# Performance work log

Measured on AMD Instinct MI355X. Metric: run time of the kernel, lower is better.

The kernel has to match this reference:

```python
import jax, jax.numpy as jnp
import numpy as np

N = 50000      # nodes
E = 800000     # edges (avg degree 16)
IN = 128       # in_feats
HID = 32       # hidden_feats per head
H = 4          # num_heads
NEG_SLOPE = 0.2


def setup_inputs() -> dict:
    key = jax.random.key(0)
    ks = jax.random.split(key, 13)
    x = jax.random.normal(ks[0], (N, IN), jnp.float32)
    src = jax.random.randint(ks[1], (E,), 0, N, jnp.int32)
    dst = jax.random.randint(ks[2], (E,), 0, N, jnp.int32)

    def lin(k, fi, fo):
        return jax.random.normal(k, (fi, fo), jnp.float32) * (1.0 / np.sqrt(fi))

    # conv1: IN -> H*HID
    W1 = lin(ks[3], IN, H * HID)
    al1 = jax.random.normal(ks[4], (H, HID), jnp.float32) * 0.1
    ar1 = jax.random.normal(ks[5], (H, HID), jnp.float32) * 0.1
    b1 = jnp.zeros((H, HID), jnp.float32)
    # conv2: H*HID -> H*HID
    W2 = lin(ks[6], H * HID, H * HID)
    al2 = jax.random.normal(ks[7], (H, HID), jnp.float32) * 0.1
    ar2 = jax.random.normal(ks[8], (H, HID), jnp.float32) * 0.1
    b2 = jnp.zeros((H, HID), jnp.float32)
    # fc: HID -> 1
    fcW = lin(ks[9], HID, 1)
    fcb = jnp.zeros((1,), jnp.float32)
    return {"x": x, "src": src, "dst": dst,
            "W1": W1, "al1": al1, "ar1": ar1, "b1": b1,
            "W2": W2, "al2": al2, "ar2": ar2, "b2": b2,
            "fcW": fcW, "fcb": fcb}


def gat_conv(x, src, dst, W, al, ar, b):
    # x: [N, F_in] -> feat: [N, H, HID]
    feat = (x @ W).reshape(N, H, HID)
    el = jnp.sum(feat * al, axis=-1)            # [N, H]
    er = jnp.sum(feat * ar, axis=-1)            # [N, H]
    e = jax.nn.leaky_relu(el[src] + er[dst], NEG_SLOPE)  # [E, H]
    # segment softmax over incoming edges of each dst node
    m = jax.ops.segment_max(e, dst, num_segments=N)      # [N, H]
    ex = jnp.exp(e - m[dst])                              # [E, H]
    denom = jax.ops.segment_sum(ex, dst, num_segments=N)  # [N, H]
    alpha = ex / denom[dst]                                # [E, H]
    msg = feat[src] * alpha[:, :, None]                    # [E, H, HID]
    out = jax.ops.segment_sum(msg, dst, num_segments=N)   # [N, H, HID]
    return out + b[None, :, :]


def reference(x, src, dst, W1, al1, ar1, b1, W2, al2, ar2, b2, fcW, fcb):
    h = gat_conv(x, src, dst, W1, al1, ar1, b1).reshape(N, H * HID)
    h = jax.nn.relu(h)
    # dropout(0.5) is identity in eval mode
    h = gat_conv(h, src, dst, W2, al2, ar2, b2).mean(axis=1)  # [N, HID]
    return h @ fcW + fcb                                       # [N, 1]
```

## Files before the change

kernel.cpp:

```cpp
#include <hip/hip_runtime.h>
#include <hip/hip_fp16.h>

#define LEAK 0.2f
#define CAP 64
#define CS 16

static __device__ inline int swz(int c, int j) {
    int qb = j >> 3, r = j & 7;
    return c * 144 + qb * 8 + (qb >> 2) * 4 + r;
}
static __device__ inline unsigned q4(float4 v, float is) {
    int x0 = __float2int_rn(v.x * is) + 128; x0 = min(max(x0, 0), 255);
    int x1 = __float2int_rn(v.y * is) + 128; x1 = min(max(x1, 0), 255);
    int x2 = __float2int_rn(v.z * is) + 128; x2 = min(max(x2, 0), 255);
    int x3 = __float2int_rn(v.w * is) + 128; x3 = min(max(x3, 0), 255);
    return (unsigned)x0 | ((unsigned)x1 << 8) | ((unsigned)x2 << 16) | ((unsigned)x3 << 24);
}

__global__ __launch_bounds__(256) void k0(
    int* __restrict__ cnt,
    const int* __restrict__ src, const int* __restrict__ dst,
    unsigned* __restrict__ pk,
    const float* __restrict__ W2, const float* __restrict__ al2,
    const float* __restrict__ ar2, const float* __restrict__ fcW,
    const float* __restrict__ b2, float* __restrict__ WfT,
    float* __restrict__ bc, int N, int E, int zb, int pkb) {
    const int b = blockIdx.x;
    const int t = threadIdx.x;
    if (b < zb) {
        int i = b * 256 + t;
        if (i < N * (CS / 4)) ((int4*)cnt)[i] = make_int4(0, 0, 0, 0);
        return;
    }
    if (b < zb + pkb) {
        int i = (b - zb) * 256 + t;
        int e0 = i * 4;
        if (e0 + 3 < E) {
            int4 d = ((const int4*)dst)[i];
            int4 s = ((const int4*)src)[i];
            ((int4*)pk)[i] = make_int4((d.x << 16) | s.x, (d.y << 16) | s.y,
                                       (d.z << 16) | s.z, (d.w << 16) | s.w);
        } else if (e0 < E) {
            for (int e = e0; e < E; e++) pk[e] = ((unsigned)dst[e] << 16) | (unsigned)src[e];
        }
        return;
    }
    int idx = (b - zb - pkb) * 256 + t;
    if (idx < 1536) {
        int c = idx >> 7, k = idx & 127;
        int h = c & 3, sel = c >> 2;
        const float* vec = (sel == 0) ? (al2 + 32 * h)
                         : (sel == 1) ? (ar2 + 32 * h) : fcW;
        float s = 0.f;
#pragma unroll 8
        for (int m = 0; m < 32; m++) s += W2[k * 128 + 32 * h + m] * vec[m];
        WfT[c * 128 + k] = s;
    } else if (idx < 1540) {
        int h = idx - 1536;
        float s = 0.f;
        for (int m = 0; m < 32; m++) s += b2[h * 32 + m] * fcW[m];
        bc[h] = s;
    }
}

__global__ __launch_bounds__(256, 4) void k_eg(
    const float* __restrict__ X, const float* __restrict__ W,
    const float* __restrict__ al, const float* __restrict__ ar,
    float2* __restrict__ elsc2, float* __restrict__ er_nh,
    unsigned* __restrict__ fq8,
    const unsigned* __restrict__ pk,
    int* __restrict__ cnt, unsigned short* __restrict__ ell,
    int N, int E, int R, int GO, int T) {
    __shared__ float sW[32 * 128];
    __shared__ float sXT[32 * 64];
    const int b = blockIdx.x;
    const int t = threadIdx.x;
    const int o = b >> 3;
    const int g0 = (o * GO) / T;
    const bool isGemm = ((o + 1) * GO) / T > g0;

    if (!isGemm) {
        const int part = b & 7;
        const int rank = o - g0;
        const int S = (N + 7) >> 3;
        const int lo = part * S;
        const int hi = (lo + S < N) ? (lo + S) : N;
        const int per = (E + R - 1) / R;
        const int e0 = rank * per;
        const int e1 = (e0 + per < E) ? (e0 + per) : E;
        int e = e0 + t;
        for (; e + 768 < e1; e += 1024) {
            unsigned p0 = pk[e];       unsigned p1 = pk[e + 256];
            unsigned p2 = pk[e + 512]; unsigned p3 = pk[e + 768];
            int d0 = (int)(p0 >> 16), d1 = (int)(p1 >> 16);
            int d2 = (int)(p2 >> 16), d3 = (int)(p3 >> 16);
            if (d0 >= lo && d0 < hi) {
                int pos = atomicAdd(&cnt[d0 * CS], 1);
                if (pos < CAP) ell[(size_t)d0 * CAP + pos] = (unsigned short)(p0 & 0xffffu);
            }
            if (d1 >= lo && d1 < hi) {
                int pos = atomicAdd(&cnt[d1 * CS], 1);
                if (pos < CAP) ell[(size_t)d1 * CAP + pos] = (unsigned short)(p1 & 0xffffu);
            }
            if (d2 >= lo && d2 < hi) {
                int pos = atomicAdd(&cnt[d2 * CS], 1);
                if (pos < CAP) ell[(size_t)d2 * CAP + pos] = (unsigned short)(p2 & 0xffffu);
            }
            if (d3 >= lo && d3 < hi) {
                int pos = atomicAdd(&cnt[d3 * CS], 1);
                if (pos < CAP) ell[(size_t)d3 * CAP + pos] = (unsigned short)(p3 & 0xffffu);
            }
        }
        for (; e < e1; e += 256) {
            unsigned p = pk[e];
            int d = (int)(p >> 16);
            if (d >= lo && d < hi) {
                int pos = atomicAdd(&cnt[d * CS], 1);
                if (pos < CAP) ell[(size_t)d * CAP + pos] = (unsigned short)(p & 0xffffu);
            }
        }
        return;
    }

    const int tile = g0 * 8 + (b & 7);
    const int r0 = tile * 64;
    if (r0 >= N) return;
    const int tx = t & 15;
    const int ty = t >> 4;
    const float4* X4 = (const float4*)X;
    const float4* W4 = (const float4*)W;
    float4* sW4 = (float4*)sW;
    const float4* sXT4 = (const float4*)sXT;

    float4 acc[4][2];
#pragma unroll
    for (int r = 0; r < 4; r++) {
        acc[r][0] = make_float4(0.f, 0.f, 0.f, 0.f);
        acc[r][1] = make_float4(0.f, 0.f, 0.f, 0.f);
    }
    for (int ks = 0; ks < 4; ++ks) {
        if (ks) __syncthreads();
#pragma unroll
        for (int i = 0; i < 4; i++) {
            int idx = i * 256 + t;
            sW4[idx] = W4[1024 * ks + idx];
        }
#pragma unroll
        for (int i = 0; i < 2; i++) {
            int idx = i * 256 + t;
            int row = idx >> 3;
            int kq = idx & 7;
            float4 v = make_float4(0.f, 0.f, 0.f, 0.f);
            if (r0 + row < N) v = X4[(size_t)(r0 + row) * 32 + ks * 8 + kq];
            int sc = ((row >> 2) ^ kq) * 4 + (row & 3);
            sXT[(4 * kq + 0) * 64 + sc] = v.x;
            sXT[(4 * kq + 1) * 64 + sc] = v.y;
            sXT[(4 * kq + 2) * 64 + sc] = v.z;
            sXT[(4 * kq + 3) * 64 + sc] = v.w;
        }
        __syncthreads();
#pragma unroll 4
        for (int k = 0; k < 32; k++) {
            float4 w0 = sW4[k * 32 + tx];
            float4 w1 = sW4[k * 32 + 16 + tx];
            float4 x0 = sXT4[k * 16 + (ty ^ (k >> 2))];
            float xs[4] = {x0.x, x0.y, x0.z, x0.w};
#pragma unroll
            for (int r = 0; r < 4; r++) {
                acc[r][0].x += xs[r] * w0.x; acc[r][0].y += xs[r] * w0.y;
                acc[r][0].z += xs[r] * w0.z; acc[r][0].w += xs[r] * w0.w;
                acc[r][1].x += xs[r] * w1.x; acc[r][1].y += xs[r] * w1.y;
                acc[r][1].z += xs[r] * w1.z; acc[r][1].w += xs[r] * w1.w;
            }
        }
    }
    const float4* al4p = (const float4*)al;
    const float4* ar4p = (const float4*)ar;
    float4 alA = al4p[tx], alB = al4p[16 + tx];
    float4 arA = ar4p[tx], arB = ar4p[16 + tx];
#pragma unroll
    for (int r = 0; r < 4; r++) {
        int row = r0 + ty * 4 + r;
        bool ok = row < N;
        float4 a0 = acc[r][0], a1 = acc[r][1];
        float m = fmaxf(fmaxf(fmaxf(fabsf(a0.x), fabsf(a0.y)),
                              fmaxf(fabsf(a0.z), fabsf(a0.w))),
                        fmaxf(fmaxf(fabsf(a1.x), fabsf(a1.y)),
                              fmaxf(fabsf(a1.z), fabsf(a1.w))));
#pragma unroll
        for (int off = 1; off < 16; off <<= 1) m = fmaxf(m, __shfl_xor(m, off));
        float scale = m * (1.f / 127.f);
        float is = (m > 0.f) ? (127.f / m) : 0.f;
        if (ok) {
            fq8[(size_t)row * 32 + tx] = q4(a0, is);
            fq8[(size_t)row * 32 + 16 + tx] = q4(a1, is);
        }
        float elA = a0.x * alA.x + a0.y * alA.y + a0.z * alA.z + a0.w * alA.w;
        float erA = a0.x * arA.x + a0.y * arA.y + a0.z * arA.z + a0.w * arA.w;
        float elB = a1.x * alB.x + a1.y * alB.y + a1.z * alB.z + a1.w * alB.w;
        float erB = a1.x * arB.x + a1.y * arB.y + a1.z * arB.z + a1.w * arB.w;
#pragma unroll
        for (int off = 1; off < 8; off <<= 1) {
            elA += __shfl_xor(elA, off); erA += __shfl_xor(erA, off);
            elB += __shfl_xor(elB, off); erB += __shfl_xor(erB, off);
        }
        if (ok && tx == 0) {
            elsc2[row * 4 + 0] = make_float2(elA, scale);
            elsc2[row * 4 + 2] = make_float2(elB, scale);
            er_nh[row * 4 + 0] = erA;
            er_nh[row * 4 + 2] = erB;
        }
        if (ok && tx == 8) {
            elsc2[row * 4 + 1] = make_float2(elA, scale);
            elsc2[row * 4 + 3] = make_float2(elB, scale);
            er_nh[row * 4 + 1] = erA;
            er_nh[row * 4 + 3] = erB;
        }
    }
}

__global__ __launch_bounds__(256) void k_agg1P(
    const unsigned* __restrict__ fq8, const float2* __restrict__ elsc2,
    const float* __restrict__ er_nh, const unsigned short* __restrict__ ell,
    const int* __restrict__ cnt, const float* __restrict__ b1,
    const float* __restrict__ WfT, float2* __restrict__ Pag,
    float* __restrict__ er2, int N) {
    __shared__ float sWf[12 * 144];
    for (int i = threadIdx.x; i < 1536; i += 256)
        sWf[swz(i >> 7, i & 127)] = WfT[i];
    __syncthreads();
    const int wave = threadIdx.x >> 6, lane = threadIdx.x & 63;
    const int nsub = lane >> 4, q = lane & 15, h = q >> 2;
    const int wbase = q * 8 + (q >> 2) * 4;
    const uint2* fq2 = (const uint2*)fq8;

    const int n = blockIdx.x * 16 + wave * 4 + nsub;
    const bool nok = n < N;
    const int nc = nok ? n : (N - 1);
    int deg = nok ? cnt[nc * CS] : 0; if (deg > CAP) deg = CAP;
    float er = nok ? er_nh[nc * 4 + h] : 0.f;
    const unsigned short* row = ell + (size_t)nc * CAP;
    uint2 rv = ((const uint2*)row)[q];

    float acc[8] = {0.f, 0.f, 0.f, 0.f, 0.f, 0.f, 0.f, 0.f};
    float den = 0.f, wss = 0.f;
    for (int j0 = 0; j0 < deg; j0 += 8) {
        int sv[8]; float2 esv[8]; uint2 fv[8];
#pragma unroll
        for (int v = 0; v < 8; v++) {
            int wrd = __shfl((int)((v & 2) ? rv.y : rv.x),
                             (lane & 48) | ((j0 >> 2) + (v >> 2)));
            int s = (v & 1) ? ((wrd >> 16) & 0xffff) : (wrd & 0xffff);
            sv[v] = (j0 + v < deg) ? s : 0;
        }
#pragma unroll
        for (int v = 0; v < 8; v++) esv[v] = elsc2[sv[v] * 4 + h];
#pragma unroll
        for (int v = 0; v < 8; v++) fv[v] = fq2[(size_t)sv[v] * 16 + q];
#pragma unroll
        for (int v = 0; v < 8; v++) {
            bool valid = (j0 + v) < deg;
            float e = esv[v].x + er;
            e = fmaxf(e, LEAK * e);
            float w = valid ? __expf(e) : 0.f;
            float ws = w * esv[v].y;
            unsigned ua = fv[v].x, ub = fv[v].y;
            acc[0] += ws * (float)(ua & 0xff);
            acc[1] += ws * (float)((ua >> 8) & 0xff);
            acc[2] += ws * (float)((ua >> 16) & 0xff);
            acc[3] += ws * (float)(ua >> 24);
            acc[4] += ws * (float)(ub & 0xff);
            acc[5] += ws * (float)((ub >> 8) & 0xff);
            acc[6] += ws * (float)((ub >> 16) & 0xff);
            acc[7] += ws * (float)(ub >> 24);
            den += w; wss += ws;
        }
    }
    float inv = (den > 0.f) ? (1.f / den) : 0.f;
    float off128 = 128.f * wss;
    float4 b1a = ((const float4*)b1)[q * 2];
    float4 b1b = ((const float4*)b1)[q * 2 + 1];
    float hv[8];
    hv[0] = fmaxf((acc[0] - off128) * inv + b1a.x, 0.f);
    hv[1] = fmaxf((acc[1] - off128) * inv + b1a.y, 0.f);
    hv[2] = fmaxf((acc[2] - off128) * inv + b1a.z, 0.f);
    hv[3] = fmaxf((acc[3] - off128) * inv + b1a.w, 0.f);
    hv[4] = fmaxf((acc[4] - off128) * inv + b1b.x, 0.f);
    hv[5] = fmaxf((acc[5] - off128) * inv + b1b.y, 0.f);
    hv[6] = fmaxf((acc[6] - off128) * inv + b1b.z, 0.f);
    hv[7] = fmaxf((acc[7] - off128) * inv + b1b.w, 0.f);
    float p[12];
#pragma unroll
    for (int c = 0; c < 12; c++) {
        const float* wr = sWf + c * 144 + wbase;
        float4 wa = *(const float4*)wr;
        float4 wb = *(const float4*)(wr + 4);
        p[c] = hv[0] * wa.x + hv[1] * wa.y + hv[2] * wa.z + hv[3] * wa.w
             + hv[4] * wb.x + hv[5] * wb.y + hv[6] * wb.z + hv[7] * wb.w;
    }
#pragma unroll
    for (int off = 1; off < 16; off <<= 1) {
#pragma unroll
        for (int c = 0; c < 12; c++) p[c] += __shfl_xor(p[c], off);
    }
    if (nok) {
        if (q < 4) Pag[(size_t)n * 4 + q] = make_float2(p[q], p[8 + q]);
        else if (q < 8) er2[(size_t)n * 4 + (q - 4)] = p[q];
    }
}

__global__ __launch_bounds__(256) void k_agg2(
    const float2* __restrict__ Pag, const float* __restrict__ er2,
    const unsigned short* __restrict__ ell, const int* __restrict__ cnt,
    const float* __restrict__ bc, const float* __restrict__ fcb,
    float* __restrict__ out, int N) {
    int idx = blockIdx.x * 256 + threadIdx.x;
    int n = idx >> 2, h = idx & 3;
    if (n >= N) return;
    int deg = cnt[n * CS]; if (deg > CAP) deg = CAP;
    float er = er2[(size_t)n * 4 + h];
    const uint4* row4 = (const uint4*)(ell + (size_t)n * CAP);
    uint4 rv[8];
#pragma unroll
    for (int i = 0; i < 8; i++) rv[i] = row4[i];

    float num = 0.f, den = 0.f;
#pragma unroll
    for (int b8 = 0; b8 < 8; ++b8) {
        int j0 = b8 * 8;
        if (j0 >= deg) break;
        int sv[8];
#pragma unroll
        for (int v = 0; v < 8; v++) {
            unsigned wrd = ((v >> 1) == 0) ? rv[b8].x
                         : ((v >> 1) == 1) ? rv[b8].y
                         : ((v >> 1) == 2) ? rv[b8].z : rv[b8].w;
            int s = (v & 1) ? (int)(wrd >> 16) : (int)(wrd & 0xffffu);
            sv[v] = (j0 + v < deg) ? s : 0;
        }
        float2 g[8];
#pragma unroll
        for (int v = 0; v < 8; v++) g[v] = Pag[(size_t)sv[v] * 4 + h];
#pragma unroll
        for (int v = 0; v < 8; v++) {
            if (j0 + v < deg) {
                float e = g[v].x + er; e = fmaxf(e, LEAK * e);
                float w = __expf(e);
                num += w * g[v].y; den += w;
            }
        }
    }
    float r = (den > 0.f) ? (num / den) : 0.f;
    r += bc[h];
    r += __shfl_xor(r, 1);
    r += __shfl_xor(r, 2);
    if (h == 0) out[n] = 0.25f * r + fcb[0];
}

extern "C" void kernel_launch(void* const* d_in, const int* in_sizes, int n_in,
                              void* d_out, int out_size, void* d_ws, size_t ws_size,
                              hipStream_t stream) {
    const float* x   = (const float*)d_in[0];
    const int* src   = (const int*)d_in[1];
    const int* dst   = (const int*)d_in[2];
    const float* W1  = (const float*)d_in[3];
    const float* al1 = (const float*)d_in[4];
    const float* ar1 = (const float*)d_in[5];
    const float* b1  = (const float*)d_in[6];
    const float* W2  = (const float*)d_in[7];
    const float* al2 = (const float*)d_in[8];
    const float* ar2 = (const float*)d_in[9];
    const float* b2  = (const float*)d_in[10];
    const float* fcW = (const float*)d_in[11];
    const float* fcb = (const float*)d_in[12];
    float* out = (float*)d_out;

    const int N = in_sizes[0] / 128;
    const int E = in_sizes[1];

    char* w = (char*)d_ws;
    size_t off = 0;
    auto alloc = [&](size_t bytes) {
        void* p = w + off;
        off = (off + bytes + 255) & ~(size_t)255;
        return p;
    };
    unsigned* fq8  = (unsigned*)alloc((size_t)N * 32 * 4);
    float2* elsc2  = (float2*)alloc((size_t)N * 4 * 8);
    float* er_nh   = (float*)alloc((size_t)N * 4 * 4);
    float2* Pag    = (float2*)alloc((size_t)N * 4 * 8);
    float* er2     = (float*)alloc((size_t)N * 4 * 4);
    float* WfT     = (float*)alloc((size_t)(12 * 128 + 4) * 4);
    float* bc      = WfT + 12 * 128;
    int* cnt       = (int*)alloc((size_t)N * CS * 4);
    unsigned short* ell = (unsigned short*)alloc((size_t)N * CAP * 2);
    unsigned* pk   = (unsigned*)alloc((size_t)E * 4);

    const int zb = (N * (CS / 4) + 255) / 256;
    const int pkb = (E / 4 + 255) / 256;
    const int gtiles = (N + 63) / 64;
    const int R = 256;
    const int GO = (gtiles + 7) / 8;
    const int T = R + GO;

    k0<<<zb + pkb + 8, 256, 0, stream>>>(
        cnt, src, dst, pk, W2, al2, ar2, fcW, b2, WfT, bc, N, E, zb, pkb);
    k_eg<<<8 * T, 256, 0, stream>>>(
        x, W1, al1, ar1, elsc2, er_nh, fq8,
        pk, cnt, ell, N, E, R, GO, T);
    k_agg1P<<<(N + 15) / 16, 256, 0, stream>>>(
        fq8, elsc2, er_nh, ell, cnt, b1, WfT, Pag, er2, N);
    k_agg2<<<(N * 4 + 255) / 256, 256, 0, stream>>>(
        Pag, er2, ell, cnt, bc, fcb, out, N);
}
```

Measured before the change: 186.5 us.

## Software-pipeline gathers in aggregation kernels and halve GEMM K-slab LDS

Both aggregation kernels now double-buffer their neighbor gathers, issuing the loads for the next chunk of 8 edges before computing on the current chunk so gather latency overlaps arithmetic. The layer-1 GEMM in k_eg moves from 4 K-steps of 32 to 8 K-steps of 16, halving its shared-memory footprint so more blocks can be resident. The prefetch doubles the register arrays, which may lower occupancy, and the smaller K-steps add extra __syncthreads barriers.

```diff
diff --git a/kernel.cpp b/kernel.cpp
--- a/kernel.cpp
+++ b/kernel.cpp
@@ -71,8 +71,8 @@
     const unsigned* __restrict__ pk,
     int* __restrict__ cnt, unsigned short* __restrict__ ell,
     int N, int E, int R, int GO, int T) {
-    __shared__ float sW[32 * 128];
-    __shared__ float sXT[32 * 64];
+    __shared__ float sW[16 * 128];
+    __shared__ float sXT[16 * 64];
     const int b = blockIdx.x;
     const int t = threadIdx.x;
     const int o = b >> 3;
@@ -138,20 +138,18 @@
         acc[r][0] = make_float4(0.f, 0.f, 0.f, 0.f);
         acc[r][1] = make_float4(0.f, 0.f, 0.f, 0.f);
     }
-    for (int ks = 0; ks < 4; ++ks) {
+    for (int ks = 0; ks < 8; ++ks) {
         if (ks) __syncthreads();
-#pragma unroll
-        for (int i = 0; i < 4; i++) {
-            int idx = i * 256 + t;
-            sW4[idx] = W4[1024 * ks + idx];
-        }
 #pragma unroll
         for (int i = 0; i < 2; i++) {
             int idx = i * 256 + t;
-            int row = idx >> 3;
-            int kq = idx & 7;
+            sW4[idx] = W4[512 * ks + idx];
+        }
+        {
+            int row = t >> 2;
+            int kq = t & 3;
             float4 v = make_float4(0.f, 0.f, 0.f, 0.f);
-            if (r0 + row < N) v = X4[(size_t)(r0 + row) * 32 + ks * 8 + kq];
+            if (r0 + row < N) v = X4[(size_t)(r0 + row) * 32 + ks * 4 + kq];
             int sc = ((row >> 2) ^ kq) * 4 + (row & 3);
             sXT[(4 * kq + 0) * 64 + sc] = v.x;
             sXT[(4 * kq + 1) * 64 + sc] = v.y;
@@ -160,7 +158,7 @@
         }
         __syncthreads();
 #pragma unroll 4
-        for (int k = 0; k < 32; k++) {
+        for (int k = 0; k < 16; k++) {
             float4 w0 = sW4[k * 32 + tx];
             float4 w1 = sW4[k * 32 + 16 + tx];
             float4 x0 = sXT4[k * 16 + (ty ^ (k >> 2))];
@@ -244,27 +242,37 @@
 
     float acc[8] = {0.f, 0.f, 0.f, 0.f, 0.f, 0.f, 0.f, 0.f};
     float den = 0.f, wss = 0.f;
-    for (int j0 = 0; j0 < deg; j0 += 8) {
-        int sv[8]; float2 esv[8]; uint2 fv[8];
+    int sv[2][8]; float2 esv[2][8]; uint2 fv[2][8];
+
+#define A1_FETCH(B, S)                                                        \
+    {                                                                         \
+        _Pragma("unroll")                                                     \
+        for (int v = 0; v < 8; v++) {                                         \
+            int wrd = __shfl((int)((v & 2) ? rv.y : rv.x),                    \
+                             (lane & 48) | ((B) * 2 + (v >> 2)));             \
+            int s = (v & 1) ? ((wrd >> 16) & 0xffff) : (wrd & 0xffff);        \
+            sv[S][v] = ((B) * 8 + v < deg) ? s : 0;                           \
+        }                                                                     \
+        _Pragma("unroll")                                                     \
+        for (int v = 0; v < 8; v++) esv[S][v] = elsc2[sv[S][v] * 4 + h];      \
+        _Pragma("unroll")                                                     \
+        for (int v = 0; v < 8; v++) fv[S][v] = fq2[(size_t)sv[S][v] * 16 + q];\
+    }
+
+    if (deg > 0) A1_FETCH(0, 0)
+#pragma unroll
+    for (int bb = 0; bb < 8; ++bb) {
+        if (bb * 8 >= deg) break;
+        const int cur = bb & 1;
+        if ((bb + 1) * 8 < deg) A1_FETCH(bb + 1, cur ^ 1)
 #pragma unroll
         for (int v = 0; v < 8; v++) {
-            int wrd = __shfl((int)((v & 2) ? rv.y : rv.x),
-                             (lane & 48) | ((j0 >> 2) + (v >> 2)));
-            int s = (v & 1) ? ((wrd >> 16) & 0xffff) : (wrd & 0xffff);
-            sv[v] = (j0 + v < deg) ? s : 0;
-        }
-#pragma unroll
-        for (int v = 0; v < 8; v++) esv[v] = elsc2[sv[v] * 4 + h];
-#pragma unroll
-        for (int v = 0; v < 8; v++) fv[v] = fq2[(size_t)sv[v] * 16 + q];
-#pragma unroll
-        for (int v = 0; v < 8; v++) {
-            bool valid = (j0 + v) < deg;
-            float e = esv[v].x + er;
+            bool valid = (bb * 8 + v) < deg;
+            float e = esv[cur][v].x + er;
             e = fmaxf(e, LEAK * e);
             float w = valid ? __expf(e) : 0.f;
-            float ws = w * esv[v].y;
-            unsigned ua = fv[v].x, ub = fv[v].y;
+            float ws = w * esv[cur][v].y;
+            unsigned ua = fv[cur][v].x, ub = fv[cur][v].y;
             acc[0] += ws * (float)(ua & 0xff);
             acc[1] += ws * (float)((ua >> 8) & 0xff);
             acc[2] += ws * (float)((ua >> 16) & 0xff);
@@ -276,6 +284,7 @@
             den += w; wss += ws;
         }
     }
+#undef A1_FETCH
     float inv = (den > 0.f) ? (1.f / den) : 0.f;
     float off128 = 128.f * wss;
     float4 b1a = ((const float4*)b1)[q * 2];
@@ -325,31 +334,38 @@
     for (int i = 0; i < 8; i++) rv[i] = row4[i];
 
     float num = 0.f, den = 0.f;
+    int sv[2][8]; float2 g[2][8];
+
+#define A2_FETCH(B, S)                                                        \
+    {                                                                         \
+        _Pragma("unroll")                                                     \
+        for (int v = 0; v < 8; v++) {                                         \
+            unsigned wrd = ((v >> 1) == 0) ? rv[B].x                          \
+                         : ((v >> 1) == 1) ? rv[B].y                          \
+                         : ((v >> 1) == 2) ? rv[B].z : rv[B].w;               \
+            int s = (v & 1) ? (int)(wrd >> 16) : (int)(wrd & 0xffffu);        \
+            sv[S][v] = ((B) * 8 + v < deg) ? s : 0;                           \
+        }                                                                     \
+        _Pragma("unroll")                                                     \
+        for (int v = 0; v < 8; v++) g[S][v] = Pag[(size_t)sv[S][v] * 4 + h];  \
+    }
+
+    if (deg > 0) A2_FETCH(0, 0)
 #pragma unroll
     for (int b8 = 0; b8 < 8; ++b8) {
-        int j0 = b8 * 8;
-        if (j0 >= deg) break;
-        int sv[8];
+        if (b8 * 8 >= deg) break;
+        const int cur = b8 & 1;
+        if ((b8 + 1) * 8 < deg) A2_FETCH(b8 + 1, cur ^ 1)
 #pragma unroll
         for (int v = 0; v < 8; v++) {
-            unsigned wrd = ((v >> 1) == 0) ? rv[b8].x
-                         : ((v >> 1) == 1) ? rv[b8].y
-                         : ((v >> 1) == 2) ? rv[b8].z : rv[b8].w;
-            int s = (v & 1) ? (int)(wrd >> 16) : (int)(wrd & 0xffffu);
-            sv[v] = (j0 + v < deg) ? s : 0;
-        }
-        float2 g[8];
-#pragma unroll
-        for (int v = 0; v < 8; v++) g[v] = Pag[(size_t)sv[v] * 4 + h];
-#pragma unroll
-        for (int v = 0; v < 8; v++) {
-            if (j0 + v < deg) {
-                float e = g[v].x + er; e = fmaxf(e, LEAK * e);
+            if (b8 * 8 + v < deg) {
+                float e = g[cur][v].x + er; e = fmaxf(e, LEAK * e);
                 float w = __expf(e);
-                num += w * g[v].y; den += w;
-            }
-        }
-    }
+                num += w * g[cur][v].y; den += w;
+            }
+        }
+    }
+#undef A2_FETCH
     float r = (den > 0.f) ? (num / den) : 0.f;
     r += bc[h];
     r += __shfl_xor(r, 1);
```

New measurement: 188.5 us. No clear change (+1.0%).

## Bucket edges by destination partition before ELL build; halve GEMM K-tile

Applied to the files above, without the earlier changes.

Replaces the filter-scan ELL build, where each of 8 partitions scanned all edges and discarded most, with a counting sort. A histogram pass in k0, a single-block scan and a scatter kernel bucket packed edges by destination partition, so each partition reads only its own edges. The edge-worker count R drops from 256 to 96. The GEMM K-chunk shrinks from 32 to 16, halving shared memory so more blocks can be resident. This adds two extra kernel launches and a serial single-block scan step.

```diff
diff --git a/kernel.cpp b/kernel.cpp
--- a/kernel.cpp
+++ b/kernel.cpp
@@ -4,6 +4,7 @@
 #define LEAK 0.2f
 #define CAP 64
 #define CS 16
+#define EPB 4096
 
 static __device__ inline int swz(int c, int j) {
     int qb = j >> 3, r = j & 7;
@@ -19,12 +20,12 @@
 
 __global__ __launch_bounds__(256) void k0(
     int* __restrict__ cnt,
-    const int* __restrict__ src, const int* __restrict__ dst,
-    unsigned* __restrict__ pk,
+    const int* __restrict__ dst, int* __restrict__ hist,
     const float* __restrict__ W2, const float* __restrict__ al2,
     const float* __restrict__ ar2, const float* __restrict__ fcW,
     const float* __restrict__ b2, float* __restrict__ WfT,
-    float* __restrict__ bc, int N, int E, int zb, int pkb) {
+    float* __restrict__ bc, int N, int E, int S, int zb, int hb) {
+    __shared__ int lh[8];
     const int b = blockIdx.x;
     const int t = threadIdx.x;
     if (b < zb) {
@@ -32,20 +33,33 @@
         if (i < N * (CS / 4)) ((int4*)cnt)[i] = make_int4(0, 0, 0, 0);
         return;
     }
-    if (b < zb + pkb) {
-        int i = (b - zb) * 256 + t;
-        int e0 = i * 4;
-        if (e0 + 3 < E) {
-            int4 d = ((const int4*)dst)[i];
-            int4 s = ((const int4*)src)[i];
-            ((int4*)pk)[i] = make_int4((d.x << 16) | s.x, (d.y << 16) | s.y,
-                                       (d.z << 16) | s.z, (d.w << 16) | s.w);
-        } else if (e0 < E) {
-            for (int e = e0; e < E; e++) pk[e] = ((unsigned)dst[e] << 16) | (unsigned)src[e];
-        }
+    if (b < zb + hb) {
+        const int blk = b - zb;
+        if (t < 8) lh[t] = 0;
+        __syncthreads();
+        const int e0 = blk * EPB;
+        const int qbase = e0 / 4;
+        const int4* dst4 = (const int4*)dst;
+#pragma unroll
+        for (int k = 0; k < 4; k++) {
+            int q = qbase + t + k * 256;
+            int eq = q * 4;
+            if (eq + 3 < E && eq < e0 + EPB) {
+                int4 d = dst4[q];
+                atomicAdd(&lh[d.x / S], 1);
+                atomicAdd(&lh[d.y / S], 1);
+                atomicAdd(&lh[d.z / S], 1);
+                atomicAdd(&lh[d.w / S], 1);
+            } else if (eq < E && eq < e0 + EPB) {
+                for (int e = eq; e < E && e < e0 + EPB; e++)
+                    atomicAdd(&lh[dst[e] / S], 1);
+            }
+        }
+        __syncthreads();
+        if (t < 8) hist[blk * 8 + t] = lh[t];
         return;
     }
-    int idx = (b - zb - pkb) * 256 + t;
+    int idx = (b - zb - hb) * 256 + t;
     if (idx < 1536) {
         int c = idx >> 7, k = idx & 127;
         int h = c & 3, sel = c >> 2;
@@ -63,16 +77,84 @@
     }
 }
 
+__global__ __launch_bounds__(256) void kscan(
+    const int* __restrict__ hist, int* __restrict__ blockBase,
+    int* __restrict__ seg, int nb, int E) {
+    __shared__ int sc[256];
+    const int t = threadIdx.x;
+    int base = 0;
+    for (int p = 0; p < 8; p++) {
+        int v = (t < nb) ? hist[t * 8 + p] : 0;
+        int x = v;
+        sc[t] = x;
+        __syncthreads();
+        for (int off = 1; off < 256; off <<= 1) {
+            int y = (t >= off) ? sc[t - off] : 0;
+            __syncthreads();
+            x += y;
+            sc[t] = x;
+            __syncthreads();
+        }
+        int tot = sc[255];
+        if (t < nb) blockBase[t * 8 + p] = base + (x - v);
+        if (t == 0) seg[p] = base;
+        base += tot;
+        __syncthreads();
+    }
+    if (t == 0) seg[8] = base;
+}
+
+__global__ __launch_bounds__(256) void kscat(
+    const int* __restrict__ src, const int* __restrict__ dst,
+    const int* __restrict__ blockBase, unsigned* __restrict__ pkb,
+    int E, int S) {
+    __shared__ int sBase[8];
+    __shared__ int lcnt[8];
+    const int blk = blockIdx.x;
+    const int t = threadIdx.x;
+    if (t < 8) { sBase[t] = blockBase[blk * 8 + t]; lcnt[t] = 0; }
+    __syncthreads();
+    const int e0 = blk * EPB;
+    const int qbase = e0 / 4;
+    const int4* dst4 = (const int4*)dst;
+    const int4* src4 = (const int4*)src;
+#pragma unroll
+    for (int k = 0; k < 4; k++) {
+        int q = qbase + t + k * 256;
+        int eq = q * 4;
+        if (eq + 3 < E && eq < e0 + EPB) {
+            int4 d = dst4[q];
+            int4 s = src4[q];
+            int p0 = d.x / S, p1 = d.y / S, p2 = d.z / S, p3 = d.w / S;
+            int r0 = atomicAdd(&lcnt[p0], 1);
+            int r1 = atomicAdd(&lcnt[p1], 1);
+            int r2 = atomicAdd(&lcnt[p2], 1);
+            int r3 = atomicAdd(&lcnt[p3], 1);
+            pkb[sBase[p0] + r0] = ((unsigned)d.x << 16) | (unsigned)s.x;
+            pkb[sBase[p1] + r1] = ((unsigned)d.y << 16) | (unsigned)s.y;
+            pkb[sBase[p2] + r2] = ((unsigned)d.z << 16) | (unsigned)s.z;
+            pkb[sBase[p3] + r3] = ((unsigned)d.w << 16) | (unsigned)s.w;
+        } else if (eq < E && eq < e0 + EPB) {
+            for (int e = eq; e < E && e < e0 + EPB; e++) {
+                int d = dst[e], s = src[e];
+                int p = d / S;
+                int r = atomicAdd(&lcnt[p], 1);
+                pkb[sBase[p] + r] = ((unsigned)d << 16) | (unsigned)s;
+            }
+        }
+    }
+}
+
 __global__ __launch_bounds__(256, 4) void k_eg(
     const float* __restrict__ X, const float* __restrict__ W,
     const float* __restrict__ al, const float* __restrict__ ar,
     float2* __restrict__ elsc2, float* __restrict__ er_nh,
     unsigned* __restrict__ fq8,
-    const unsigned* __restrict__ pk,
+    const unsigned* __restrict__ pkb, const int* __restrict__ seg,
     int* __restrict__ cnt, unsigned short* __restrict__ ell,
     int N, int E, int R, int GO, int T) {
-    __shared__ float sW[32 * 128];
-    __shared__ float sXT[32 * 64];
+    __shared__ float sW[16 * 128];
+    __shared__ float sXT[16 * 64];
     const int b = blockIdx.x;
     const int t = threadIdx.x;
     const int o = b >> 3;
@@ -82,42 +164,32 @@
     if (!isGemm) {
         const int part = b & 7;
         const int rank = o - g0;
-        const int S = (N + 7) >> 3;
-        const int lo = part * S;
-        const int hi = (lo + S < N) ? (lo + S) : N;
-        const int per = (E + R - 1) / R;
-        const int e0 = rank * per;
-        const int e1 = (e0 + per < E) ? (e0 + per) : E;
+        const int s0 = seg[part];
+        const int s1 = seg[part + 1];
+        const int len = s1 - s0;
+        const int per = (len + R - 1) / R;
+        const int e0 = s0 + rank * per;
+        const int e1 = (e0 + per < s1) ? (e0 + per) : s1;
         int e = e0 + t;
         for (; e + 768 < e1; e += 1024) {
-            unsigned p0 = pk[e];       unsigned p1 = pk[e + 256];
-            unsigned p2 = pk[e + 512]; unsigned p3 = pk[e + 768];
+            unsigned p0 = pkb[e];       unsigned p1 = pkb[e + 256];
+            unsigned p2 = pkb[e + 512]; unsigned p3 = pkb[e + 768];
             int d0 = (int)(p0 >> 16), d1 = (int)(p1 >> 16);
             int d2 = (int)(p2 >> 16), d3 = (int)(p3 >> 16);
-            if (d0 >= lo && d0 < hi) {
-                int pos = atomicAdd(&cnt[d0 * CS], 1);
-                if (pos < CAP) ell[(size_t)d0 * CAP + pos] = (unsigned short)(p0 & 0xffffu);
-            }
-            if (d1 >= lo && d1 < hi) {
-                int pos = atomicAdd(&cnt[d1 * CS], 1);
-                if (pos < CAP) ell[(size_t)d1 * CAP + pos] = (unsigned short)(p1 & 0xffffu);
-            }
-            if (d2 >= lo && d2 < hi) {
-                int pos = atomicAdd(&cnt[d2 * CS], 1);
-                if (pos < CAP) ell[(size_t)d2 * CAP + pos] = (unsigned short)(p2 & 0xffffu);
-            }
-            if (d3 >= lo && d3 < hi) {
-                int pos = atomicAdd(&cnt[d3 * CS], 1);
-                if (pos < CAP) ell[(size_t)d3 * CAP + pos] = (unsigned short)(p3 & 0xffffu);
-            }
+            int q0 = atomicAdd(&cnt[d0 * CS], 1);
+            if (q0 < CAP) ell[(size_t)d0 * CAP + q0] = (unsigned short)(p0 & 0xffffu);
+            int q1 = atomicAdd(&cnt[d1 * CS], 1);
+            if (q1 < CAP) ell[(size_t)d1 * CAP + q1] = (unsigned short)(p1 & 0xffffu);
+            int q2 = atomicAdd(&cnt[d2 * CS], 1);
+            if (q2 < CAP) ell[(size_t)d2 * CAP + q2] = (unsigned short)(p2 & 0xffffu);
+            int q3 = atomicAdd(&cnt[d3 * CS], 1);
+            if (q3 < CAP) ell[(size_t)d3 * CAP + q3] = (unsigned short)(p3 & 0xffffu);
         }
         for (; e < e1; e += 256) {
-            unsigned p = pk[e];
+            unsigned p = pkb[e];
             int d = (int)(p >> 16);
-            if (d >= lo && d < hi) {
-                int pos = atomicAdd(&cnt[d * CS], 1);
-                if (pos < CAP) ell[(size_t)d * CAP + pos] = (unsigned short)(p & 0xffffu);
-            }
+            int q = atomicAdd(&cnt[d * CS], 1);
+            if (q < CAP) ell[(size_t)d * CAP + q] = (unsigned short)(p & 0xffffu);
         }
         return;
     }
@@ -138,20 +210,18 @@
         acc[r][0] = make_float4(0.f, 0.f, 0.f, 0.f);
         acc[r][1] = make_float4(0.f, 0.f, 0.f, 0.f);
     }
-    for (int ks = 0; ks < 4; ++ks) {
+    for (int ks = 0; ks < 8; ++ks) {
         if (ks) __syncthreads();
-#pragma unroll
-        for (int i = 0; i < 4; i++) {
-            int idx = i * 256 + t;
-            sW4[idx] = W4[1024 * ks + idx];
-        }
 #pragma unroll
         for (int i = 0; i < 2; i++) {
             int idx = i * 256 + t;
-            int row = idx >> 3;
-            int kq = idx & 7;
+            sW4[idx] = W4[512 * ks + idx];
+        }
+        {
+            int row = t >> 2;
+            int kq = t & 3;
             float4 v = make_float4(0.f, 0.f, 0.f, 0.f);
-            if (r0 + row < N) v = X4[(size_t)(r0 + row) * 32 + ks * 8 + kq];
+            if (r0 + row < N) v = X4[(size_t)(r0 + row) * 32 + ks * 4 + kq];
             int sc = ((row >> 2) ^ kq) * 4 + (row & 3);
             sXT[(4 * kq + 0) * 64 + sc] = v.x;
             sXT[(4 * kq + 1) * 64 + sc] = v.y;
@@ -160,7 +230,7 @@
         }
         __syncthreads();
 #pragma unroll 4
-        for (int k = 0; k < 32; k++) {
+        for (int k = 0; k < 16; k++) {
             float4 w0 = sW4[k * 32 + tx];
             float4 w1 = sW4[k * 32 + 16 + tx];
             float4 x0 = sXT4[k * 16 + (ty ^ (k >> 2))];
@@ -377,6 +447,7 @@
 
     const int N = in_sizes[0] / 128;
     const int E = in_sizes[1];
+    const int S = (N + 7) / 8;
 
     char* w = (char*)d_ws;
     size_t off = 0;
@@ -394,20 +465,25 @@
     float* bc      = WfT + 12 * 128;
     int* cnt       = (int*)alloc((size_t)N * CS * 4);
     unsigned short* ell = (unsigned short*)alloc((size_t)N * CAP * 2);
-    unsigned* pk   = (unsigned*)alloc((size_t)E * 4);
+    unsigned* pkb  = (unsigned*)alloc((size_t)E * 4);
+    const int nb   = (E + EPB - 1) / EPB;
+    int* hist      = (int*)alloc((size_t)nb * 8 * 4);
+    int* blockBase = (int*)alloc((size_t)nb * 8 * 4);
+    int* seg       = (int*)alloc(9 * 4);
 
     const int zb = (N * (CS / 4) + 255) / 256;
-    const int pkb = (E / 4 + 255) / 256;
     const int gtiles = (N + 63) / 64;
-    const int R = 256;
+    const int R = 96;
     const int GO = (gtiles + 7) / 8;
     const int T = R + GO;
 
-    k0<<<zb + pkb + 8, 256, 0, stream>>>(
-        cnt, src, dst, pk, W2, al2, ar2, fcW, b2, WfT, bc, N, E, zb, pkb);
+    k0<<<zb + nb + 8, 256, 0, stream>>>(
+        cnt, dst, hist, W2, al2, ar2, fcW, b2, WfT, bc, N, E, S, zb, nb);
+    kscan<<<1, 256, 0, stream>>>(hist, blockBase, seg, nb, E);
+    kscat<<<nb, 256, 0, stream>>>(src, dst, blockBase, pkb, E, S);
     k_eg<<<8 * T, 256, 0, stream>>>(
         x, W1, al1, ar1, elsc2, er_nh, fq8,
-        pk, cnt, ell, N, E, R, GO, T);
+        pkb, seg, cnt, ell, N, E, R, GO, T);
     k_agg1P<<<(N + 15) / 16, 256, 0, stream>>>(
         fq8, elsc2, er_nh, ell, cnt, b1, WfT, Pag, er2, N);
     k_agg2<<<(N * 4 + 255) / 256, 256, 0, stream>>>(
```

New measurement: 207.9 us. +11.5%, slower.

## Fuse ELL build and GEMM tile into every block, halve shared k-chunk

Applied to the files above, without the earlier changes.

The combined kernel previously gave each block either an edge-bucketing (ELL build) role or a 64-row GEMM role. Now every block first does its share of the bucketing and then, if its index is below the tile count, also computes one GEMM tile. This removes the separate GEMM blocks and the role-assignment arithmetic. The GEMM shared-memory staging is also cut from a 32-wide k chunk to a 16-wide chunk over eight iterations, halving shared memory per block to allow higher occupancy. The trade-off is that GEMM work now waits behind each block's atomic-heavy bucketing, and there are twice as many barrier-separated staging rounds.

```diff
diff --git a/kernel.cpp b/kernel.cpp
--- a/kernel.cpp
+++ b/kernel.cpp
@@ -63,25 +63,22 @@
     }
 }
 
-__global__ __launch_bounds__(256, 4) void k_eg(
+__global__ __launch_bounds__(256, 4) void k_egc(
     const float* __restrict__ X, const float* __restrict__ W,
     const float* __restrict__ al, const float* __restrict__ ar,
     float2* __restrict__ elsc2, float* __restrict__ er_nh,
     unsigned* __restrict__ fq8,
     const unsigned* __restrict__ pk,
     int* __restrict__ cnt, unsigned short* __restrict__ ell,
-    int N, int E, int R, int GO, int T) {
-    __shared__ float sW[32 * 128];
-    __shared__ float sXT[32 * 64];
+    int N, int E, int R, int gtiles) {
+    __shared__ float sW[16 * 128];
+    __shared__ float sXT[16 * 64];
     const int b = blockIdx.x;
     const int t = threadIdx.x;
-    const int o = b >> 3;
-    const int g0 = (o * GO) / T;
-    const bool isGemm = ((o + 1) * GO) / T > g0;
-
-    if (!isGemm) {
+
+    {
         const int part = b & 7;
-        const int rank = o - g0;
+        const int rank = b >> 3;
         const int S = (N + 7) >> 3;
         const int lo = part * S;
         const int hi = (lo + S < N) ? (lo + S) : N;
@@ -95,36 +92,34 @@
             int d0 = (int)(p0 >> 16), d1 = (int)(p1 >> 16);
             int d2 = (int)(p2 >> 16), d3 = (int)(p3 >> 16);
             if (d0 >= lo && d0 < hi) {
-                int pos = atomicAdd(&cnt[d0 * CS], 1);
-                if (pos < CAP) ell[(size_t)d0 * CAP + pos] = (unsigned short)(p0 & 0xffffu);
+                int q0 = atomicAdd(&cnt[d0 * CS], 1);
+                if (q0 < CAP) ell[(size_t)d0 * CAP + q0] = (unsigned short)(p0 & 0xffffu);
             }
             if (d1 >= lo && d1 < hi) {
-                int pos = atomicAdd(&cnt[d1 * CS], 1);
-                if (pos < CAP) ell[(size_t)d1 * CAP + pos] = (unsigned short)(p1 & 0xffffu);
+                int q1 = atomicAdd(&cnt[d1 * CS], 1);
+                if (q1 < CAP) ell[(size_t)d1 * CAP + q1] = (unsigned short)(p1 & 0xffffu);
             }
             if (d2 >= lo && d2 < hi) {
-                int pos = atomicAdd(&cnt[d2 * CS], 1);
-                if (pos < CAP) ell[(size_t)d2 * CAP + pos] = (unsigned short)(p2 & 0xffffu);
+                int q2 = atomicAdd(&cnt[d2 * CS], 1);
+                if (q2 < CAP) ell[(size_t)d2 * CAP + q2] = (unsigned short)(p2 & 0xffffu);
             }
             if (d3 >= lo && d3 < hi) {
-                int pos = atomicAdd(&cnt[d3 * CS], 1);
-                if (pos < CAP) ell[(size_t)d3 * CAP + pos] = (unsigned short)(p3 & 0xffffu);
+                int q3 = atomicAdd(&cnt[d3 * CS], 1);
+                if (q3 < CAP) ell[(size_t)d3 * CAP + q3] = (unsigned short)(p3 & 0xffffu);
             }
         }
         for (; e < e1; e += 256) {
             unsigned p = pk[e];
             int d = (int)(p >> 16);
             if (d >= lo && d < hi) {
-                int pos = atomicAdd(&cnt[d * CS], 1);
-                if (pos < CAP) ell[(size_t)d * CAP + pos] = (unsigned short)(p & 0xffffu);
-            }
-        }
-        return;
-    }
-
-    const int tile = g0 * 8 + (b & 7);
-    const int r0 = tile * 64;
-    if (r0 >= N) return;
+                int q = atomicAdd(&cnt[d * CS], 1);
+                if (q < CAP) ell[(size_t)d * CAP + q] = (unsigned short)(p & 0xffffu);
+            }
+        }
+    }
+    if (b >= gtiles) return;
+
+    const int r0 = b * 64;
     const int tx = t & 15;
     const int ty = t >> 4;
     const float4* X4 = (const float4*)X;
@@ -138,20 +133,18 @@
         acc[r][0] = make_float4(0.f, 0.f, 0.f, 0.f);
         acc[r][1] = make_float4(0.f, 0.f, 0.f, 0.f);
     }
-    for (int ks = 0; ks < 4; ++ks) {
+    for (int ks = 0; ks < 8; ++ks) {
         if (ks) __syncthreads();
-#pragma unroll
-        for (int i = 0; i < 4; i++) {
-            int idx = i * 256 + t;
-            sW4[idx] = W4[1024 * ks + idx];
-        }
 #pragma unroll
         for (int i = 0; i < 2; i++) {
             int idx = i * 256 + t;
-            int row = idx >> 3;
-            int kq = idx & 7;
+            sW4[idx] = W4[512 * ks + idx];
+        }
+        {
+            int row = t >> 2;
+            int kq = t & 3;
             float4 v = make_float4(0.f, 0.f, 0.f, 0.f);
-            if (r0 + row < N) v = X4[(size_t)(r0 + row) * 32 + ks * 8 + kq];
+            if (r0 + row < N) v = X4[(size_t)(r0 + row) * 32 + ks * 4 + kq];
             int sc = ((row >> 2) ^ kq) * 4 + (row & 3);
             sXT[(4 * kq + 0) * 64 + sc] = v.x;
             sXT[(4 * kq + 1) * 64 + sc] = v.y;
@@ -160,7 +153,7 @@
         }
         __syncthreads();
 #pragma unroll 4
-        for (int k = 0; k < 32; k++) {
+        for (int k = 0; k < 16; k++) {
             float4 w0 = sW4[k * 32 + tx];
             float4 w1 = sW4[k * 32 + 16 + tx];
             float4 x0 = sXT4[k * 16 + (ty ^ (k >> 2))];
@@ -400,14 +393,12 @@
     const int pkb = (E / 4 + 255) / 256;
     const int gtiles = (N + 63) / 64;
     const int R = 256;
-    const int GO = (gtiles + 7) / 8;
-    const int T = R + GO;
 
     k0<<<zb + pkb + 8, 256, 0, stream>>>(
         cnt, src, dst, pk, W2, al2, ar2, fcW, b2, WfT, bc, N, E, zb, pkb);
-    k_eg<<<8 * T, 256, 0, stream>>>(
+    k_egc<<<8 * R, 256, 0, stream>>>(
         x, W1, al1, ar1, elsc2, er_nh, fq8,
-        pk, cnt, ell, N, E, R, GO, T);
+        pk, cnt, ell, N, E, R, gtiles);
     k_agg1P<<<(N + 15) / 16, 256, 0, stream>>>(
         fq8, elsc2, er_nh, ell, cnt, b1, WfT, Pag, er2, N);
     k_agg2<<<(N * 4 + 255) / 256, 256, 0, stream>>>(
```

Result: slower. 191.5 us (+2.7%).
